# Performance work log

Hardware: AMD Instinct MI355X
Metric: run time of the kernel (lower is better)

## Reference

```python
import jax, jax.numpy as jnp
import numpy as np

N_NODES = 100000
N_EDGES = 1600000
IN_FEAT = 128
OUT_FEAT = 64
RRELU_SLOPE = (1.0 / 8.0 + 1.0 / 3.0) / 2.0  # nn.RReLU eval-mode slope = 11/48


def setup_inputs() -> dict:
    key = jax.random.key(0)
    k1, k2, k3, k4, k5 = jax.random.split(key, 5)
    feat = jax.random.normal(k1, (N_NODES, IN_FEAT), dtype=jnp.float32)
    src = jax.random.randint(k2, (N_EDGES,), 0, N_NODES, dtype=jnp.int64)
    dst = jax.random.randint(k3, (N_EDGES,), 0, N_NODES, dtype=jnp.int64)
    # xavier-uniform-ish init
    b1 = np.sqrt(6.0 / (IN_FEAT + OUT_FEAT))
    b2 = np.sqrt(6.0 / (OUT_FEAT + OUT_FEAT))
    w1 = jax.random.uniform(k4, (IN_FEAT, OUT_FEAT), jnp.float32, -b1, b1)
    w2 = jax.random.uniform(k5, (OUT_FEAT, OUT_FEAT), jnp.float32, -b2, b2)
    return {"feat": feat, "src": src, "dst": dst, "w1": w1, "w2": w2}


def _gather_sum(h, src, dst):
    # DGL copy_src('h','m') + sum: for each dst node, sum messages from src nodes
    return jax.ops.segment_sum(h[src], dst, num_segments=N_NODES)


def _rrelu(x):
    return jnp.where(x >= 0, x, RRELU_SLOPE * x)


def reference(feat, src, dst, w1, w2):
    # pattern = 0: linear -> gather -> rrelu, linear -> gather -> rrelu
    h = feat @ w1                      # [N, out_feat]
    h = _gather_sum(h, src, dst)       # [N, out_feat]
    h = _rrelu(h)
    h = h @ w2                         # [N, out_feat]
    h = _gather_sum(h, src, dst)       # [N, out_feat]
    h = _rrelu(h)
    return h
```

## Files before the change

### kernel.cpp

```cpp
#include <hip/hip_runtime.h>

#define N_NODES 100000
#define N_EDGES 1600000
#define IN_FEAT 128
#define OUT_FEAT 64
#define SLOPE 0.22916666666666666f

#define NPB 128
#define NB 782
#define CAP 2560
#define BIN_CHUNK 8192
#define EPT 32
#define BIN_BLOCKS ((N_EDGES + BIN_CHUNK - 1) / BIN_CHUNK)
#define GEMM1_BLOCKS (N_NODES / 16)
#define WTS 68
#define LS 136

typedef __attribute__((ext_vector_type(8))) short short8;
typedef __attribute__((ext_vector_type(4))) float f32x4;

__device__ __forceinline__ ushort f2bf(float x) {
    unsigned u = __float_as_uint(x);
    u += 0x7FFFu + ((u >> 16) & 1u);
    return (ushort)(u >> 16);
}

union FatSmem {
    struct { ushort a[16 * LS]; ushort b[64 * LS]; } g;
    struct { int cnt[NB]; int gbase[NB]; } bb;
};

__global__ __launch_bounds__(256) void gemm1_binning_kernel(
        const float* __restrict__ feat, const float* __restrict__ w1,
        ushort* __restrict__ h1,
        const int* __restrict__ src, const int* __restrict__ dst,
        int* __restrict__ bcur, int* __restrict__ pairs) {
    __shared__ FatSmem s;
    const int tid = threadIdx.x;

    if (blockIdx.x >= BIN_BLOCKS) {
        const int row0 = (blockIdx.x - BIN_BLOCKS) * 16;

        {
            const float4* fg = (const float4*)(feat + (size_t)row0 * IN_FEAT);
#pragma unroll
            for (int half = 0; half < 2; ++half) {
                const int i = tid + half * 256;
                const float4 v = fg[i];
                const int r = i >> 5;
                const int c4 = (i & 31) * 4;
                ushort* p = s.g.a + r * LS + c4;
                ushort4 u;
                u.x = f2bf(v.x); u.y = f2bf(v.y); u.z = f2bf(v.z); u.w = f2bf(v.w);
                *(ushort4*)p = u;
            }
        }
        {
            const int c = tid & 63;
            const int kb = tid >> 6;
#pragma unroll
            for (int j2 = 0; j2 < 16; ++j2) {
                const int k = kb * 32 + j2 * 2;
                const float lo = w1[(size_t)k * OUT_FEAT + c];
                const float hi = w1[(size_t)(k + 1) * OUT_FEAT + c];
                const unsigned pk = (unsigned)f2bf(lo) | ((unsigned)f2bf(hi) << 16);
                *(unsigned*)(s.g.b + c * LS + k) = pk;
            }
        }
        __syncthreads();

        const int w = tid >> 6;
        const int l = tid & 63;
        const int lr = l & 15;
        const int lk = l >> 4;

        f32x4 acc = {0.f, 0.f, 0.f, 0.f};
        const char* Ab = (const char*)s.g.a;
        const char* Bb = (const char*)(s.g.b + (w * 16 + lr) * LS);
#pragma unroll
        for (int kk = 0; kk < 4; ++kk) {
            const short8 af = *(const short8*)(Ab + lr * (LS * 2) + kk * 64 + lk * 16);
            const short8 bf = *(const short8*)(Bb + kk * 64 + lk * 16);
            acc = __builtin_amdgcn_mfma_f32_16x16x32_bf16(af, bf, acc, 0, 0, 0);
        }

#pragma unroll
        for (int i = 0; i < 4; ++i) {
            const int row = lk * 4 + i;
            h1[(size_t)(row0 + row) * OUT_FEAT + w * 16 + lr] = f2bf(acc[i]);
        }
    } else {
        int* cnt = s.bb.cnt;
        int* gbase = s.bb.gbase;
        for (int i = tid; i < NB; i += 256) cnt[i] = 0;
        __syncthreads();
        const int base = blockIdx.x * BIN_CHUNK;
        int bl[EPT];
        int vp[EPT];
#pragma unroll
        for (int i = 0; i < EPT; ++i) {
            const int e = base + i * 256 + tid;
            if (e < N_EDGES) {
                const int d = dst[e];
                const int b = d >> 7;
                const int lpos = atomicAdd(&cnt[b], 1);
                bl[i] = (b << 13) | lpos;
                vp[i] = ((d & 127) << 17) | src[e];
            } else {
                bl[i] = -1;
            }
        }
        __syncthreads();
        for (int i = tid; i < NB; i += 256) {
            const int cc = cnt[i];
            gbase[i] = cc ? (i * CAP + atomicAdd(&bcur[i], cc)) : 0;
        }
        __syncthreads();
#pragma unroll
        for (int i = 0; i < EPT; ++i) {
            if (bl[i] >= 0) {
                const int b = bl[i] >> 13, lpos = bl[i] & 8191;
                pairs[gbase[b] + lpos] = vp[i];
            }
        }
    }
}

__global__ __launch_bounds__(256) void sort2_kernel(const int* __restrict__ pairs,
                                                    const int* __restrict__ bcur,
                                                    int* __restrict__ csr,
                                                    int2* __restrict__ nseg) {
    __shared__ int cnt[NPB];
    __shared__ int cur[NPB];
    __shared__ int wtot;
    const int b = blockIdx.x;
    const int t = threadIdx.x;
    const int beg = b * CAP;
    const int end = beg + bcur[b];
    if (t < NPB) cnt[t] = 0;
    __syncthreads();
    for (int i = beg + t; i < end; i += 256)
        atomicAdd(&cnt[pairs[i] >> 17], 1);
    __syncthreads();
    int v = 0, x = 0;
    const int lane = t & 63, w = t >> 6;
    if (t < NPB) {
        v = cnt[t];
        x = v;
#pragma unroll
        for (int off = 1; off < 64; off <<= 1) {
            int y = __shfl_up(x, off);
            if (lane >= off) x += y;
        }
        if (t == 63) wtot = x;
    }
    __syncthreads();
    if (t < NPB) {
        const int gp = beg + (x - v) + (w ? wtot : 0);
        cur[t] = gp;
        nseg[b * NPB + t] = make_int2(gp, gp + v);
    }
    __syncthreads();
    for (int i = beg + t; i < end; i += 256) {
        const int p = pairs[i];
        const int pos = atomicAdd(&cur[p >> 17], 1);
        csr[pos] = (p & 0x1FFFF) << 7;
    }
}

__device__ __forceinline__ float2 gather_pairs(const char* __restrict__ hb,
                                               const int* __restrict__ csr,
                                               int beg, int end, int hi, int cp4) {
    float ax = 0.f, ay = 0.f;
    int i = beg;
#define LOADU(k) const unsigned u##k = *(const unsigned*)(hb + (unsigned)(csr[i + 2*(k) + hi] + cp4))
#define ACCU(k)                                            \
    ax += __uint_as_float(u##k << 16);                     \
    ay += __uint_as_float(u##k & 0xFFFF0000u)
    for (; i + 16 <= end; i += 16) {
        LOADU(0); LOADU(1); LOADU(2); LOADU(3);
        LOADU(4); LOADU(5); LOADU(6); LOADU(7);
        ACCU(0); ACCU(1); ACCU(2); ACCU(3);
        ACCU(4); ACCU(5); ACCU(6); ACCU(7);
    }
    if (i + 8 <= end) {
        LOADU(0); LOADU(1); LOADU(2); LOADU(3);
        ACCU(0); ACCU(1); ACCU(2); ACCU(3);
        i += 8;
    }
    if (i + 4 <= end) {
        LOADU(0); LOADU(1);
        ACCU(0); ACCU(1);
        i += 4;
    }
    for (; i < end; i += 2) {
        if (i + hi < end) {
            const unsigned u = *(const unsigned*)(hb + (unsigned)(csr[i + hi] + cp4));
            ax += __uint_as_float(u << 16);
            ay += __uint_as_float(u & 0xFFFF0000u);
        }
    }
#undef LOADU
#undef ACCU
    return make_float2(ax, ay);
}

__global__ __launch_bounds__(256) void agg_gemm2_kernel(const ushort* __restrict__ h,
                                                        const int* __restrict__ csr,
                                                        const int2* __restrict__ nseg,
                                                        const float* __restrict__ w2,
                                                        ushort* __restrict__ h2) {
    __shared__ float wt[OUT_FEAT * WTS];
    __shared__ float rowbuf[4][OUT_FEAT];
    const int tid = threadIdx.x;
    const int c = tid & 63;

    {
        const int kb = tid >> 6;
#pragma unroll
        for (int j = 0; j < 16; ++j) {
            const int k = kb * 16 + j;
            wt[c * WTS + k] = w2[k * OUT_FEAT + c];
        }
    }
    __syncthreads();

    const int wv = tid >> 6;
    const int hi = (tid >> 5) & 1, cp = tid & 31;
    const int node = blockIdx.x * 4 + wv;
    const int2 seg = nseg[node];
    const int beg = __builtin_amdgcn_readfirstlane(seg.x);
    const int end = __builtin_amdgcn_readfirstlane(seg.y);

    float2 acc = gather_pairs((const char*)h, csr, beg, end, hi, cp * 4);
    acc.x += __shfl_xor(acc.x, 32);
    acc.y += __shfl_xor(acc.y, 32);
    acc.x = acc.x >= 0.f ? acc.x : acc.x * SLOPE;
    acc.y = acc.y >= 0.f ? acc.y : acc.y * SLOPE;

    if (hi == 0) ((float2*)rowbuf[wv])[cp] = acc;

    float o = 0.f;
    const float4* rb4 = (const float4*)rowbuf[wv];
    const float4* wt4 = (const float4*)(wt + c * WTS);
#pragma unroll
    for (int j4 = 0; j4 < 16; ++j4) {
        const float4 r = rb4[j4];
        const float4 v = wt4[j4];
        o += r.x * v.x + r.y * v.y + r.z * v.z + r.w * v.w;
    }
    h2[(size_t)node * OUT_FEAT + c] = f2bf(o);
}

__global__ __launch_bounds__(256) void agg_rrelu_kernel(const ushort* __restrict__ h,
                                                        const int* __restrict__ csr,
                                                        const int2* __restrict__ nseg,
                                                        float* __restrict__ out) {
    const int tid = threadIdx.x;
    const int hi = (tid >> 5) & 1, cp = tid & 31;
    const int node = blockIdx.x * 4 + (tid >> 6);
    const int2 seg = nseg[node];
    const int beg = __builtin_amdgcn_readfirstlane(seg.x);
    const int end = __builtin_amdgcn_readfirstlane(seg.y);

    float2 acc = gather_pairs((const char*)h, csr, beg, end, hi, cp * 4);
    acc.x += __shfl_xor(acc.x, 32);
    acc.y += __shfl_xor(acc.y, 32);
    if (hi == 0) {
        acc.x = acc.x >= 0.f ? acc.x : acc.x * SLOPE;
        acc.y = acc.y >= 0.f ? acc.y : acc.y * SLOPE;
        ((float2*)(out + (size_t)node * OUT_FEAT))[cp] = acc;
    }
}

extern "C" void kernel_launch(void* const* d_in, const int* in_sizes, int n_in,
                              void* d_out, int out_size, void* d_ws, size_t ws_size,
                              hipStream_t stream) {
    const float* feat = (const float*)d_in[0];
    const int*   src  = (const int*)d_in[1];
    const int*   dst  = (const int*)d_in[2];
    const float* w1   = (const float*)d_in[3];
    const float* w2   = (const float*)d_in[4];
    float* out = (float*)d_out;

    ushort* h1   = (ushort*)d_ws;
    ushort* h2   = h1 + (size_t)N_NODES * OUT_FEAT;
    int*    pairs = (int*)h2;
    int*    csr  = (int*)(h2 + (size_t)N_NODES * OUT_FEAT);
    int2*   nseg = (int2*)(csr + NB * CAP);
    int*    bcur = (int*)(nseg + NB * NPB);

    hipMemsetAsync(bcur, 0, NB * sizeof(int), stream);
    gemm1_binning_kernel<<<BIN_BLOCKS + GEMM1_BLOCKS, 256, 0, stream>>>(
        feat, w1, h1, src, dst, bcur, pairs);
    sort2_kernel<<<NB, 256, 0, stream>>>(pairs, bcur, csr, nseg);

    agg_gemm2_kernel<<<N_NODES / 4, 256, 0, stream>>>(h1, csr, nseg, w2, h2);

    agg_rrelu_kernel<<<N_NODES / 4, 256, 0, stream>>>(h2, csr, nseg, out);
}
```

Baseline: 150.9 us.

## Pretranspose weights in a single init kernel and widen sort block

Adds a one-block init kernel that zeroes the bin counters, stores W1 transposed as bf16 and stores W2 transposed and padded. The memset is no longer needed. GEMM1 blocks now read B fragments straight from global memory instead of staging them through LDS, and the agg_gemm2 blocks load the pre-padded W2 with float4 copies. The sort kernel uses 512 threads per block. This removes redundant per-block weight transposition across thousands of blocks. The cost is an extra serial launch of a single-block kernel and uncoalesced-ish global B reads, which should be served from cache.

Result: slower. 160.7 us (+6.5%).

```diff
diff --git a/kernel.cpp b/kernel.cpp
--- a/kernel.cpp
+++ b/kernel.cpp
@@ -15,6 +15,7 @@
 #define GEMM1_BLOCKS (N_NODES / 16)
 #define WTS 68
 #define LS 136
+#define STH 512
 
 typedef __attribute__((ext_vector_type(8))) short short8;
 typedef __attribute__((ext_vector_type(4))) float f32x4;
@@ -25,13 +26,30 @@
     return (ushort)(u >> 16);
 }
 
+__global__ __launch_bounds__(256) void init_kernel(const float* __restrict__ w1,
+                                                   const float* __restrict__ w2,
+                                                   int* __restrict__ bcur,
+                                                   ushort* __restrict__ w1t,
+                                                   float* __restrict__ w2t) {
+    const int tid = threadIdx.x;
+    for (int i = tid; i < NB; i += 256) bcur[i] = 0;
+    for (int i = tid; i < OUT_FEAT * IN_FEAT; i += 256) {
+        const int c = i >> 7, k = i & 127;
+        w1t[i] = f2bf(w1[(size_t)k * OUT_FEAT + c]);
+    }
+    for (int i = tid; i < OUT_FEAT * WTS; i += 256) {
+        const int c = i / WTS, k = i - c * WTS;
+        w2t[i] = (k < OUT_FEAT) ? w2[(size_t)k * OUT_FEAT + c] : 0.f;
+    }
+}
+
 union FatSmem {
-    struct { ushort a[16 * LS]; ushort b[64 * LS]; } g;
+    struct { ushort a[16 * LS]; } g;
     struct { int cnt[NB]; int gbase[NB]; } bb;
 };
 
 __global__ __launch_bounds__(256) void gemm1_binning_kernel(
-        const float* __restrict__ feat, const float* __restrict__ w1,
+        const float* __restrict__ feat, const ushort* __restrict__ w1t,
         ushort* __restrict__ h1,
         const int* __restrict__ src, const int* __restrict__ dst,
         int* __restrict__ bcur, int* __restrict__ pairs) {
@@ -55,18 +73,6 @@
                 *(ushort4*)p = u;
             }
         }
-        {
-            const int c = tid & 63;
-            const int kb = tid >> 6;
-#pragma unroll
-            for (int j2 = 0; j2 < 16; ++j2) {
-                const int k = kb * 32 + j2 * 2;
-                const float lo = w1[(size_t)k * OUT_FEAT + c];
-                const float hi = w1[(size_t)(k + 1) * OUT_FEAT + c];
-                const unsigned pk = (unsigned)f2bf(lo) | ((unsigned)f2bf(hi) << 16);
-                *(unsigned*)(s.g.b + c * LS + k) = pk;
-            }
-        }
         __syncthreads();
 
         const int w = tid >> 6;
@@ -76,11 +82,11 @@
 
         f32x4 acc = {0.f, 0.f, 0.f, 0.f};
         const char* Ab = (const char*)s.g.a;
-        const char* Bb = (const char*)(s.g.b + (w * 16 + lr) * LS);
+        const ushort* Brow = w1t + (w * 16 + lr) * IN_FEAT;
 #pragma unroll
         for (int kk = 0; kk < 4; ++kk) {
             const short8 af = *(const short8*)(Ab + lr * (LS * 2) + kk * 64 + lk * 16);
-            const short8 bf = *(const short8*)(Bb + kk * 64 + lk * 16);
+            const short8 bf = *(const short8*)(Brow + kk * 32 + lk * 8);
             acc = __builtin_amdgcn_mfma_f32_16x16x32_bf16(af, bf, acc, 0, 0, 0);
         }
 
@@ -126,7 +132,7 @@
     }
 }
 
-__global__ __launch_bounds__(256) void sort2_kernel(const int* __restrict__ pairs,
+__global__ __launch_bounds__(STH) void sort2_kernel(const int* __restrict__ pairs,
                                                     const int* __restrict__ bcur,
                                                     int* __restrict__ csr,
                                                     int2* __restrict__ nseg) {
@@ -139,7 +145,7 @@
     const int end = beg + bcur[b];
     if (t < NPB) cnt[t] = 0;
     __syncthreads();
-    for (int i = beg + t; i < end; i += 256)
+    for (int i = beg + t; i < end; i += STH)
         atomicAdd(&cnt[pairs[i] >> 17], 1);
     __syncthreads();
     int v = 0, x = 0;
@@ -161,7 +167,7 @@
         nseg[b * NPB + t] = make_int2(gp, gp + v);
     }
     __syncthreads();
-    for (int i = beg + t; i < end; i += 256) {
+    for (int i = beg + t; i < end; i += STH) {
         const int p = pairs[i];
         const int pos = atomicAdd(&cur[p >> 17], 1);
         csr[pos] = (p & 0x1FFFF) << 7;
@@ -208,7 +214,7 @@
 __global__ __launch_bounds__(256) void agg_gemm2_kernel(const ushort* __restrict__ h,
                                                         const int* __restrict__ csr,
                                                         const int2* __restrict__ nseg,
-                                                        const float* __restrict__ w2,
+                                                        const float* __restrict__ w2t,
                                                         ushort* __restrict__ h2) {
     __shared__ float wt[OUT_FEAT * WTS];
     __shared__ float rowbuf[4][OUT_FEAT];
@@ -216,12 +222,11 @@
     const int c = tid & 63;
 
     {
-        const int kb = tid >> 6;
-#pragma unroll
-        for (int j = 0; j < 16; ++j) {
-            const int k = kb * 16 + j;
-            wt[c * WTS + k] = w2[k * OUT_FEAT + c];
-        }
+        const float4* g4 = (const float4*)w2t;
+        float4* l4 = (float4*)wt;
+#pragma unroll
+        for (int j = 0; j < 4; ++j) l4[tid + j * 256] = g4[tid + j * 256];
+        if (tid < 64) l4[1024 + tid] = g4[1024 + tid];
     }
     __syncthreads();
 
@@ -289,13 +294,16 @@
     int*    csr  = (int*)(h2 + (size_t)N_NODES * OUT_FEAT);
     int2*   nseg = (int2*)(csr + NB * CAP);
     int*    bcur = (int*)(nseg + NB * NPB);
-
-    hipMemsetAsync(bcur, 0, NB * sizeof(int), stream);
+    ushort* w1t  = (ushort*)(bcur + NB);
+    float*  w2t  = (float*)(w1t + OUT_FEAT * IN_FEAT);
+
+    init_kernel<<<1, 256, 0, stream>>>(w1, w2, bcur, w1t, w2t);
+
     gemm1_binning_kernel<<<BIN_BLOCKS + GEMM1_BLOCKS, 256, 0, stream>>>(
-        feat, w1, h1, src, dst, bcur, pairs);
-    sort2_kernel<<<NB, 256, 0, stream>>>(pairs, bcur, csr, nseg);
-
-    agg_gemm2_kernel<<<N_NODES / 4, 256, 0, stream>>>(h1, csr, nseg, w2, h2);
+        feat, w1t, h1, src, dst, bcur, pairs);
+    sort2_kernel<<<NB, STH, 0, stream>>>(pairs, bcur, csr, nseg);
+
+    agg_gemm2_kernel<<<N_NODES / 4, 256, 0, stream>>>(h1, csr, nseg, w2t, h2);
 
     agg_rrelu_kernel<<<N_NODES / 4, 256, 0, stream>>>(h2, csr, nseg, out);
 }
```
